# Kernel optimization log

Hardware: AMD Instinct MI355X
Metric: run time of the kernel (lower is better)

The kernel has to match this reference:

```python
import jax, jax.numpy as jnp
import numpy as np

H = 512
S = 65  # 64 board cells + appended constant 1


def _heads(y, wk, wq, wv):
    # y: [H, S]; wk/wq/wv: [3, H, H] -> atts: [3, S, H]
    def one(wk_i, wq_i, wv_i):
        k = wk_i @ y            # [H, S]
        q = wq_i @ y            # [H, S]
        v = wv_i @ y            # [H, S]
        sm = jax.nn.softmax(k.T @ q, axis=1)  # [S, S], softmax over dim=1
        return sm @ v.T         # [S, H]
    return jax.vmap(one)(wk, wq, wv)


def setup_inputs() -> dict:
    key = jax.random.key(0)
    ks = jax.random.split(key, 10)
    r = lambda k, s: jax.random.normal(k, s, dtype=jnp.float32)
    return {
        "inputs": r(ks[0], (1, 64)),
        "embedding": r(ks[1], (H, S)),
        "wq": r(ks[2], (3, 3, H, H)),
        "wk": r(ks[3], (3, 3, H, H)),
        "wv": r(ks[4], (3, 3, H, H)),
        "linear1": r(ks[5], (3 * H, H)),
        "linear2": r(ks[6], (3 * H, H)),
        "linear3": r(ks[7], (3 * H, 2 * H)),
        "linear4": r(ks[8], (2 * H, H)),
        "linear5": r(ks[9], (H, 64)),
    }


def reference(inputs, embedding, wq, wk, wv, linear1, linear2, linear3, linear4, linear5):
    x = jnp.concatenate([inputs[0], jnp.ones((1,), inputs.dtype)])  # [S]
    y = embedding * x  # [H, S] (broadcast over rows)

    # Layer 1 (3 heads)
    a1 = _heads(y, wk[0], wq[0], wv[0])  # [3, S, H]
    y = jax.nn.relu(jnp.concatenate([a1[0], a1[1], a1[2]], axis=1) @ linear1).T  # [H, S]

    # Layer 2 -- NOTE: original code cats att11, att12, att23 (a bug we preserve)
    a2 = _heads(y, wk[1], wq[1], wv[1])
    y = jax.nn.relu(jnp.concatenate([a1[0], a1[1], a2[2]], axis=1) @ linear2).T  # [H, S]

    # Layer 3 -- NOTE: original code cats att11, att12, att33 (preserved)
    a3 = _heads(y, wk[2], wq[2], wv[2])
    y = jax.nn.relu(jnp.concatenate([a1[0], a1[1], a3[2]], axis=1) @ linear3)[64]  # [2H]

    # dropout p=0.1 -> identity in eval mode
    y = jnp.tanh(y @ linear4)  # [H]
    score = y @ linear5        # [64]
    return score[None, :]      # [1, 64]
```

## Files before the change

kernel.cpp:

```cpp
#include <hip/hip_runtime.h>
#include <hip/hip_bf16.h>
#include <math.h>

#define H 512
#define S 65
#define SP 80
#define HS (H * S)
#define PHS (H * SP)
#define KS3 24
#define KS4 16


__global__ void scale_embed_kernel(const float* __restrict__ inp,
                                   const float* __restrict__ emb,
                                   float* __restrict__ yT) {
    int i = blockIdx.x * blockDim.x + threadIdx.x;
    if (i < PHS) {
        int s = i / H;
        int h = i % H;
        float v = 0.f;
        if (s < S) {
            float x = (s == 64) ? 1.0f : inp[s];
            v = emb[h * S + s] * x;
        }
        yT[i] = v;
    }
}

template <int COMBINE>
__global__ void __launch_bounds__(256, 1)
kqv_gemm_tiled(const float* __restrict__ wq,
               const float* __restrict__ wk,
               const float* __restrict__ wv,
               int mat0,
               const float* __restrict__ src,
               float* __restrict__ part) {
    int slot  = blockIdx.z;
    int which = blockIdx.y;
    int mat = mat0 + slot;
    const float* W = (which == 0 ? wk : (which == 1 ? wq : wv)) + (size_t)mat * H * H;

    int n0   = (blockIdx.x & 7) * 64;
    int kidx = blockIdx.x >> 3;

    __shared__ float Wt[64 * 64];
    __shared__ float As[SP * 64];

    int t  = threadIdx.x;
    int nq = t & 15;
    int g  = t >> 4;

    float4 acc[5];
#pragma unroll
    for (int r = 0; r < 5; ++r) acc[r] = make_float4(0.f, 0.f, 0.f, 0.f);

    for (int ch = 0; ch < 4; ++ch) {
        int kc0 = kidx * 256 + ch * 64;
#pragma unroll
        for (int c = 0; c < 4; ++c) {
            int f = c * 256 + t;
            int wn  = f >> 4;
            int kf4 = f & 15;
            float4 w4 = *(const float4*)(W + (size_t)(n0 + wn) * H + kc0 + 4 * kf4);
            int sw = ((wn >> 2) ^ (kf4 & 7));
            int base = (4 * kf4) * 64 + 4 * sw + (wn & 3);
            Wt[base      ] = w4.x;
            Wt[base +  64] = w4.y;
            Wt[base + 128] = w4.z;
            Wt[base + 192] = w4.w;
        }
#pragma unroll
        for (int c = 0; c < 5; ++c) {
            int f = c * 256 + t;
            int as  = f >> 4;
            int kf4 = f & 15;
            const float* addr = src + (size_t)as * H + kc0 + 4 * kf4;
            float4 v;
            if (COMBINE) {
                v = make_float4(0.f, 0.f, 0.f, 0.f);
#pragma unroll
                for (int p = 0; p < 6; ++p) {
                    float4 u = *(const float4*)(addr + (size_t)p * PHS);
                    v.x += u.x; v.y += u.y; v.z += u.z; v.w += u.w;
                }
                v.x = fmaxf(v.x, 0.f); v.y = fmaxf(v.y, 0.f);
                v.z = fmaxf(v.z, 0.f); v.w = fmaxf(v.w, 0.f);
            } else {
                v = *(const float4*)addr;
            }
            *(float4*)(&As[as * 64 + 4 * kf4]) = v;
        }
        __syncthreads();

#pragma unroll
        for (int k4 = 0; k4 < 16; ++k4) {
            int swc = 4 * (nq ^ (k4 & 7));
            float4 w0 = *(const float4*)(&Wt[(4 * k4 + 0) * 64 + swc]);
            float4 w1 = *(const float4*)(&Wt[(4 * k4 + 1) * 64 + swc]);
            float4 w2 = *(const float4*)(&Wt[(4 * k4 + 2) * 64 + swc]);
            float4 w3 = *(const float4*)(&Wt[(4 * k4 + 3) * 64 + swc]);
#pragma unroll
            for (int r = 0; r < 5; ++r) {
                float4 a = *(const float4*)(&As[(g + 16 * r) * 64 + 4 * k4]);
                acc[r].x = fmaf(a.x, w0.x, acc[r].x);
                acc[r].y = fmaf(a.x, w0.y, acc[r].y);
                acc[r].z = fmaf(a.x, w0.z, acc[r].z);
                acc[r].w = fmaf(a.x, w0.w, acc[r].w);
                acc[r].x = fmaf(a.y, w1.x, acc[r].x);
                acc[r].y = fmaf(a.y, w1.y, acc[r].y);
                acc[r].z = fmaf(a.y, w1.z, acc[r].z);
                acc[r].w = fmaf(a.y, w1.w, acc[r].w);
                acc[r].x = fmaf(a.z, w2.x, acc[r].x);
                acc[r].y = fmaf(a.z, w2.y, acc[r].y);
                acc[r].z = fmaf(a.z, w2.z, acc[r].z);
                acc[r].w = fmaf(a.z, w2.w, acc[r].w);
                acc[r].x = fmaf(a.w, w3.x, acc[r].x);
                acc[r].y = fmaf(a.w, w3.y, acc[r].y);
                acc[r].z = fmaf(a.w, w3.z, acc[r].z);
                acc[r].w = fmaf(a.w, w3.w, acc[r].w);
            }
        }
        __syncthreads();
    }

    float* P = part + (size_t)((slot * 3 + which) * 2 + kidx) * PHS;
#pragma unroll
    for (int r = 0; r < 5; ++r) {
        *(float4*)(P + (size_t)(g + 16 * r) * H + n0 + 4 * nq) = acc[r];
    }
}

__device__ __forceinline__ float score_part(const float* __restrict__ Q0,
                                            const float* __restrict__ Q1,
                                            const float* __restrict__ ka,
                                            int b, int t) {
    const float4* q0 = (const float4*)(Q0 + (size_t)b * H) + t * 32;
    const float4* q1 = (const float4*)(Q1 + (size_t)b * H) + t * 32;
    const float4* kl = (const float4*)ka + t * 32;
    float4 c0 = {0,0,0,0}, c1 = {0,0,0,0};
#pragma unroll
    for (int u = 0; u < 32; u += 2) {
        float4 qa = q0[u], qb = q1[u], k0 = kl[u];
        float4 qc = q0[u+1], qd = q1[u+1], k1 = kl[u+1];
        c0.x = fmaf(k0.x, qa.x + qb.x, c0.x);
        c0.y = fmaf(k0.y, qa.y + qb.y, c0.y);
        c0.z = fmaf(k0.z, qa.z + qb.z, c0.z);
        c0.w = fmaf(k0.w, qa.w + qb.w, c0.w);
        c1.x = fmaf(k1.x, qc.x + qd.x, c1.x);
        c1.y = fmaf(k1.y, qc.y + qd.y, c1.y);
        c1.z = fmaf(k1.z, qc.z + qd.z, c1.z);
        c1.w = fmaf(k1.w, qc.w + qd.w, c1.w);
    }
    return ((c0.x + c0.y) + (c0.z + c0.w)) + ((c1.x + c1.y) + (c1.z + c1.w));
}

__global__ void attn_kernel(const float* __restrict__ kqvp,
                            float* __restrict__ att) {
    int a = blockIdx.x;
    int slot = blockIdx.y;
    int tid = threadIdx.x;

    const float* base = kqvp + (size_t)slot * 6 * PHS;
    const float* K0 = base;
    const float* K1 = base + PHS;
    const float* Q0 = base + 2 * (size_t)PHS;
    const float* Q1 = base + 3 * (size_t)PHS;
    const float* V0 = base + 4 * (size_t)PHS;
    const float* V1 = base + 5 * (size_t)PHS;
    float* ao = att + (size_t)slot * PHS + (size_t)a * H;

    __shared__ float ka[H];
    __shared__ float sp[4 * 65];
    __shared__ float smv[S];
    __shared__ float p[S];

    ka[tid]       = K0[(size_t)a * H + tid]       + K1[(size_t)a * H + tid];
    ka[tid + 256] = K0[(size_t)a * H + tid + 256] + K1[(size_t)a * H + tid + 256];
    __syncthreads();

    {
        int b = tid & 63;
        int t = tid >> 6;
        sp[t * 65 + b] = score_part(Q0, Q1, ka, b, t);
        if (tid < 4) sp[tid * 65 + 64] = score_part(Q0, Q1, ka, 64, tid);
    }
    __syncthreads();

    if (tid < S) {
        smv[tid] = (sp[tid] + sp[65 + tid]) + (sp[130 + tid] + sp[195 + tid]);
    }
    __syncthreads();

    float maxv = -INFINITY;
    for (int i = 0; i < S; ++i) maxv = fmaxf(maxv, smv[i]);
    float sum = 0.0f;
    for (int i = 0; i < S; ++i) sum += expf(smv[i] - maxv);
    float inv = 1.0f / sum;
    if (tid < S) p[tid] = expf(smv[tid] - maxv) * inv;
    __syncthreads();

#pragma unroll
    for (int rep = 0; rep < 2; ++rep) {
        int hh = tid + rep * 256;
        float a0 = 0.f, a1 = 0.f;
#pragma unroll 4
        for (int b = 0; b < 64; b += 2) {
            a0 = fmaf(p[b    ], V0[(size_t)(b    ) * H + hh] + V1[(size_t)(b    ) * H + hh], a0);
            a1 = fmaf(p[b + 1], V0[(size_t)(b + 1) * H + hh] + V1[(size_t)(b + 1) * H + hh], a1);
        }
        a0 = fmaf(p[64], V0[(size_t)64 * H + hh] + V1[(size_t)64 * H + hh], a0);
        ao[hh] = a0 + a1;
    }
}

__global__ void mega_lin_kernel(const float* __restrict__ att1,
                                const float* __restrict__ lin1,
                                const float* __restrict__ lin2,
                                const float* __restrict__ lin3,
                                float* __restrict__ plin1,
                                float* __restrict__ plin2,
                                float* __restrict__ tpart) {
    int bx = blockIdx.x;
    int tid = threadIdx.x;

    if (bx < 1300) {
        const float* att;
        const float* L;
        float* dst;
        int x, seg;
        if (bx < 780) {
            seg = bx / 130; x = bx - seg * 130;
            att = att1 + (size_t)(seg >> 1) * PHS;
            L   = lin1 + (size_t)(seg * 256) * H;
            dst = plin1 + (size_t)seg * PHS;
        } else {
            int b2 = bx - 780;
            seg = b2 / 130; x = b2 - seg * 130;
            att = att1 + (size_t)(seg >> 1) * PHS;
            L   = lin2 + (size_t)(seg * 256) * H;
            dst = plin2 + (size_t)seg * PHS;
        }
        int i = x * 256 + tid;
        int s = i / H;
        int h = i % H;
        const float* row = att + (size_t)s * H + (seg & 1) * 256;
        const float* Lh = L + h;
        float a0 = 0.f, a1 = 0.f, a2 = 0.f, a3 = 0.f;
        for (int j = 0; j < 256; j += 4) {
            a0 = fmaf(row[j + 0], Lh[(size_t)(j + 0) * H], a0);
            a1 = fmaf(row[j + 1], Lh[(size_t)(j + 1) * H], a1);
            a2 = fmaf(row[j + 2], Lh[(size_t)(j + 2) * H], a2);
            a3 = fmaf(row[j + 3], Lh[(size_t)(j + 3) * H], a3);
        }
        dst[(size_t)s * H + h] = (a0 + a1) + (a2 + a3);
    } else {
        int idx = bx - 1300;
        int j2 = (idx & 3) * 256 + tid;
        int ks = idx >> 2;
        const float* row = att1 + (size_t)(ks >> 3) * PHS + (size_t)64 * H;
        int j0 = (ks & 7) * 64;
        int jbase = ks * 64;
        float a0 = 0.f, a1 = 0.f, a2 = 0.f, a3 = 0.f;
        for (int j = 0; j < 64; j += 4) {
            a0 = fmaf(row[j0 + j + 0], lin3[(size_t)(jbase + j + 0) * 1024 + j2], a0);
            a1 = fmaf(row[j0 + j + 1], lin3[(size_t)(jbase + j + 1) * 1024 + j2], a1);
            a2 = fmaf(row[j0 + j + 2], lin3[(size_t)(jbase + j + 2) * 1024 + j2], a2);
            a3 = fmaf(row[j0 + j + 3], lin3[(size_t)(jbase + j + 3) * 1024 + j2], a3);
        }
        tpart[ks * 1024 + j2] = (a0 + a1) + (a2 + a3);
    }
}

__global__ void lin2c_kernel(const float* __restrict__ att2,
                             const float* __restrict__ lin2,
                             float* __restrict__ plin2) {
    int seg = 4 + blockIdx.y;
    int i = blockIdx.x * 256 + threadIdx.x;
    int s = i / H;
    int h = i % H;
    const float* row = att2 + (size_t)s * H + (seg & 1) * 256;
    const float* Lh = lin2 + (size_t)(seg * 256) * H + h;
    float a0 = 0.f, a1 = 0.f, a2 = 0.f, a3 = 0.f;
    for (int j = 0; j < 256; j += 4) {
        a0 = fmaf(row[j + 0], Lh[(size_t)(j + 0) * H], a0);
        a1 = fmaf(row[j + 1], Lh[(size_t)(j + 1) * H], a1);
        a2 = fmaf(row[j + 2], Lh[(size_t)(j + 2) * H], a2);
        a3 = fmaf(row[j + 3], Lh[(size_t)(j + 3) * H], a3);
    }
    plin2[(size_t)seg * PHS + (size_t)s * H + h] = (a0 + a1) + (a2 + a3);
}

__global__ void attn3_lin3c_kernel(const float* __restrict__ kqvp,
                                   const float* __restrict__ lin3,
                                   float* __restrict__ tpart) {
    int tid = threadIdx.x;
    int ks  = 16 + blockIdx.y;
    int j2  = blockIdx.x * 256 + tid;
    int j0  = (ks & 7) * 64;

    const float* K0 = kqvp;
    const float* K1 = kqvp + PHS;
    const float* Q0 = kqvp + 2 * (size_t)PHS;
    const float* Q1 = kqvp + 3 * (size_t)PHS;
    const float* V0 = kqvp + 4 * (size_t)PHS;
    const float* V1 = kqvp + 5 * (size_t)PHS;

    __shared__ float ka[H];
    __shared__ float sp[4 * 65];
    __shared__ float smv[S];
    __shared__ float p[S];
    __shared__ float att_s[64];

    ka[tid]       = K0[(size_t)64 * H + tid]       + K1[(size_t)64 * H + tid];
    ka[tid + 256] = K0[(size_t)64 * H + tid + 256] + K1[(size_t)64 * H + tid + 256];
    __syncthreads();

    {
        int b = tid & 63;
        int t = tid >> 6;
        sp[t * 65 + b] = score_part(Q0, Q1, ka, b, t);
        if (tid < 4) sp[tid * 65 + 64] = score_part(Q0, Q1, ka, 64, tid);
    }
    __syncthreads();

    if (tid < S) {
        smv[tid] = (sp[tid] + sp[65 + tid]) + (sp[130 + tid] + sp[195 + tid]);
    }
    __syncthreads();

    float maxv = -INFINITY;
    for (int i = 0; i < S; ++i) maxv = fmaxf(maxv, smv[i]);
    float sum = 0.0f;
    for (int i = 0; i < S; ++i) sum += expf(smv[i] - maxv);
    float inv = 1.0f / sum;
    if (tid < S) p[tid] = expf(smv[tid] - maxv) * inv;
    __syncthreads();

    if (tid < 64) {
        int hh = j0 + tid;
        float a0 = 0.f, a1 = 0.f;
#pragma unroll 4
        for (int b = 0; b < 64; b += 2) {
            a0 = fmaf(p[b    ], V0[(size_t)(b    ) * H + hh] + V1[(size_t)(b    ) * H + hh], a0);
            a1 = fmaf(p[b + 1], V0[(size_t)(b + 1) * H + hh] + V1[(size_t)(b + 1) * H + hh], a1);
        }
        a0 = fmaf(p[64], V0[(size_t)64 * H + hh] + V1[(size_t)64 * H + hh], a0);
        att_s[tid] = a0 + a1;
    }
    __syncthreads();

    int jbase = ks * 64;
    float a0 = 0.f, a1 = 0.f, a2 = 0.f, a3 = 0.f;
    for (int j = 0; j < 64; j += 4) {
        a0 = fmaf(att_s[j + 0], lin3[(size_t)(jbase + j + 0) * 1024 + j2], a0);
        a1 = fmaf(att_s[j + 1], lin3[(size_t)(jbase + j + 1) * 1024 + j2], a1);
        a2 = fmaf(att_s[j + 2], lin3[(size_t)(jbase + j + 2) * 1024 + j2], a2);
        a3 = fmaf(att_s[j + 3], lin3[(size_t)(jbase + j + 3) * 1024 + j2], a3);
    }
    tpart[ks * 1024 + j2] = (a0 + a1) + (a2 + a3);
}

__global__ void lin4_partial_kernel(const float* __restrict__ tpart,
                                    const float* __restrict__ lin4,
                                    float* __restrict__ upart) {
    __shared__ float tl[64];
    int hh = blockIdx.x * 256 + threadIdx.x;
    int ks = blockIdx.y;
    int j2base = ks * 64;

    if (threadIdx.x < 64) {
        int j2 = j2base + threadIdx.x;
        float s = 0.f;
#pragma unroll
        for (int p = 0; p < KS3; ++p) s += tpart[p * 1024 + j2];
        tl[threadIdx.x] = fmaxf(s, 0.f);
    }
    __syncthreads();

    float a0 = 0.f, a1 = 0.f, a2 = 0.f, a3 = 0.f;
    for (int j = 0; j < 64; j += 4) {
        a0 = fmaf(tl[j + 0], lin4[(size_t)(j2base + j + 0) * H + hh], a0);
        a1 = fmaf(tl[j + 1], lin4[(size_t)(j2base + j + 1) * H + hh], a1);
        a2 = fmaf(tl[j + 2], lin4[(size_t)(j2base + j + 2) * H + hh], a2);
        a3 = fmaf(tl[j + 3], lin4[(size_t)(j2base + j + 3) * H + hh], a3);
    }
    upart[ks * H + hh] = (a0 + a1) + (a2 + a3);
}

__global__ void final_out_kernel(const float* __restrict__ upart,
                                 const float* __restrict__ lin5,
                                 float* __restrict__ out) {
    __shared__ float u[H];
    __shared__ float pr[8][64];
    int tid = threadIdx.x;

    {
        float s = 0.f;
#pragma unroll
        for (int p = 0; p < KS4; ++p) s += upart[p * H + tid];
        u[tid] = tanhf(s);
    }
    __syncthreads();

    int o  = tid & 63;
    int sl = tid >> 6;
    float acc = 0.f;
    int h0 = sl * 64;
#pragma unroll 8
    for (int j = 0; j < 64; ++j) {
        acc = fmaf(u[h0 + j], lin5[(h0 + j) * 64 + o], acc);
    }
    pr[sl][o] = acc;
    __syncthreads();

    if (tid < 64) {
        float s = 0.f;
#pragma unroll
        for (int p = 0; p < 8; ++p) s += pr[p][tid];
        out[tid] = s;
    }
}

extern "C" void kernel_launch(void* const* d_in, const int* in_sizes, int n_in,
                              void* d_out, int out_size, void* d_ws, size_t ws_size,
                              hipStream_t stream) {
    const float* inputs  = (const float*)d_in[0];
    const float* emb     = (const float*)d_in[1];
    const float* wq      = (const float*)d_in[2];
    const float* wk      = (const float*)d_in[3];
    const float* wv      = (const float*)d_in[4];
    const float* linear1 = (const float*)d_in[5];
    const float* linear2 = (const float*)d_in[6];
    const float* linear3 = (const float*)d_in[7];
    const float* linear4 = (const float*)d_in[8];
    const float* linear5 = (const float*)d_in[9];
    float* out = (float*)d_out;

    float* ws    = (float*)d_ws;
    float* y     = ws;
    float* kqvp  = y     + PHS;
    float* att1  = kqvp  + 18 * PHS;
    float* att2  = att1  + 3 * PHS;
    float* plin1 = att2  + PHS;
    float* plin2 = plin1 + 6 * PHS;
    float* tpart = plin2 + 6 * PHS;
    float* upart = tpart + KS3 * 1024;

    const int nbp = PHS / 256;

    scale_embed_kernel<<<nbp, 256, 0, stream>>>(inputs, emb, y);

    kqv_gemm_tiled<0><<<dim3(16, 3, 3), 256, 0, stream>>>(wq, wk, wv, 0, y, kqvp);
    attn_kernel<<<dim3(S, 3), 256, 0, stream>>>(kqvp, att1);
    mega_lin_kernel<<<1364, 256, 0, stream>>>(att1, linear1, linear2, linear3,
                                              plin1, plin2, tpart);

    kqv_gemm_tiled<1><<<dim3(16, 3, 1), 256, 0, stream>>>(wq, wk, wv, 5, plin1, kqvp);
    attn_kernel<<<dim3(S, 1), 256, 0, stream>>>(kqvp, att2);
    lin2c_kernel<<<dim3(130, 2), 256, 0, stream>>>(att2, linear2, plin2);

    kqv_gemm_tiled<1><<<dim3(16, 3, 1), 256, 0, stream>>>(wq, wk, wv, 8, plin2, kqvp);
    attn3_lin3c_kernel<<<dim3(4, 8), 256, 0, stream>>>(kqvp, linear3, tpart);

    lin4_partial_kernel<<<dim3(2, KS4), 256, 0, stream>>>(tpart, linear4, upart);
    final_out_kernel<<<1, 512, 0, stream>>>(upart, linear5, out);
}
```

Before: 260.4 us.

## Retile KQV GEMM, register-block linear projections, split out combine+relu kernel

```diff
diff --git a/kernel.cpp b/kernel.cpp
--- a/kernel.cpp
+++ b/kernel.cpp
@@ -27,107 +27,96 @@
     }
 }
 
-template <int COMBINE>
+__device__ __forceinline__ void mac4(float4& c, float ax, float ay, float az,
+                                     float aw, const float4& w0, const float4& w1,
+                                     const float4& w2, const float4& w3) {
+    c.x = fmaf(ax, w0.x, c.x); c.y = fmaf(ax, w0.y, c.y);
+    c.z = fmaf(ax, w0.z, c.z); c.w = fmaf(ax, w0.w, c.w);
+    c.x = fmaf(ay, w1.x, c.x); c.y = fmaf(ay, w1.y, c.y);
+    c.z = fmaf(ay, w1.z, c.z); c.w = fmaf(ay, w1.w, c.w);
+    c.x = fmaf(az, w2.x, c.x); c.y = fmaf(az, w2.y, c.y);
+    c.z = fmaf(az, w2.z, c.z); c.w = fmaf(az, w2.w, c.w);
+    c.x = fmaf(aw, w3.x, c.x); c.y = fmaf(aw, w3.y, c.y);
+    c.z = fmaf(aw, w3.z, c.z); c.w = fmaf(aw, w3.w, c.w);
+}
+
 __global__ void __launch_bounds__(256, 1)
 kqv_gemm_tiled(const float* __restrict__ wq,
                const float* __restrict__ wk,
                const float* __restrict__ wv,
                int mat0,
-               const float* __restrict__ src,
+               const float* __restrict__ yT,
                float* __restrict__ part) {
     int slot  = blockIdx.z;
     int which = blockIdx.y;
     int mat = mat0 + slot;
     const float* W = (which == 0 ? wk : (which == 1 ? wq : wv)) + (size_t)mat * H * H;
 
-    int n0   = (blockIdx.x & 7) * 64;
-    int kidx = blockIdx.x >> 3;
-
-    __shared__ float Wt[64 * 64];
-    __shared__ float As[SP * 64];
+    int n0   = (blockIdx.x & 15) * 32;
+    int kidx = blockIdx.x >> 4;
+
+    __shared__ float Wt[64 * 32];
+    __shared__ float As[SP * 68];
 
     int t  = threadIdx.x;
-    int nq = t & 15;
-    int g  = t >> 4;
-
-    float4 acc[5];
-#pragma unroll
-    for (int r = 0; r < 5; ++r) acc[r] = make_float4(0.f, 0.f, 0.f, 0.f);
+    int nq = t & 7;
+    int g  = t >> 3;
+    bool r2 = (g < 16);
+
+    float4 acc0 = {0,0,0,0}, acc1 = {0,0,0,0}, acc2 = {0,0,0,0};
 
     for (int ch = 0; ch < 4; ++ch) {
         int kc0 = kidx * 256 + ch * 64;
 #pragma unroll
-        for (int c = 0; c < 4; ++c) {
+        for (int c = 0; c < 2; ++c) {
             int f = c * 256 + t;
             int wn  = f >> 4;
             int kf4 = f & 15;
             float4 w4 = *(const float4*)(W + (size_t)(n0 + wn) * H + kc0 + 4 * kf4);
             int sw = ((wn >> 2) ^ (kf4 & 7));
-            int base = (4 * kf4) * 64 + 4 * sw + (wn & 3);
-            Wt[base      ] = w4.x;
-            Wt[base +  64] = w4.y;
-            Wt[base + 128] = w4.z;
-            Wt[base + 192] = w4.w;
+            int base = (4 * kf4) * 32 + 4 * sw + (wn & 3);
+            Wt[base     ] = w4.x;
+            Wt[base + 32] = w4.y;
+            Wt[base + 64] = w4.z;
+            Wt[base + 96] = w4.w;
         }
 #pragma unroll
         for (int c = 0; c < 5; ++c) {
             int f = c * 256 + t;
             int as  = f >> 4;
             int kf4 = f & 15;
-            const float* addr = src + (size_t)as * H + kc0 + 4 * kf4;
-            float4 v;
-            if (COMBINE) {
-                v = make_float4(0.f, 0.f, 0.f, 0.f);
-#pragma unroll
-                for (int p = 0; p < 6; ++p) {
-                    float4 u = *(const float4*)(addr + (size_t)p * PHS);
-                    v.x += u.x; v.y += u.y; v.z += u.z; v.w += u.w;
-                }
-                v.x = fmaxf(v.x, 0.f); v.y = fmaxf(v.y, 0.f);
-                v.z = fmaxf(v.z, 0.f); v.w = fmaxf(v.w, 0.f);
-            } else {
-                v = *(const float4*)addr;
-            }
-            *(float4*)(&As[as * 64 + 4 * kf4]) = v;
+            *(float4*)(&As[as * 68 + 4 * kf4]) =
+                *(const float4*)(yT + (size_t)as * H + kc0 + 4 * kf4);
         }
         __syncthreads();
 
 #pragma unroll
         for (int k4 = 0; k4 < 16; ++k4) {
             int swc = 4 * (nq ^ (k4 & 7));
-            float4 w0 = *(const float4*)(&Wt[(4 * k4 + 0) * 64 + swc]);
-            float4 w1 = *(const float4*)(&Wt[(4 * k4 + 1) * 64 + swc]);
-            float4 w2 = *(const float4*)(&Wt[(4 * k4 + 2) * 64 + swc]);
-            float4 w3 = *(const float4*)(&Wt[(4 * k4 + 3) * 64 + swc]);
-#pragma unroll
-            for (int r = 0; r < 5; ++r) {
-                float4 a = *(const float4*)(&As[(g + 16 * r) * 64 + 4 * k4]);
-                acc[r].x = fmaf(a.x, w0.x, acc[r].x);
-                acc[r].y = fmaf(a.x, w0.y, acc[r].y);
-                acc[r].z = fmaf(a.x, w0.z, acc[r].z);
-                acc[r].w = fmaf(a.x, w0.w, acc[r].w);
-                acc[r].x = fmaf(a.y, w1.x, acc[r].x);
-                acc[r].y = fmaf(a.y, w1.y, acc[r].y);
-                acc[r].z = fmaf(a.y, w1.z, acc[r].z);
-                acc[r].w = fmaf(a.y, w1.w, acc[r].w);
-                acc[r].x = fmaf(a.z, w2.x, acc[r].x);
-                acc[r].y = fmaf(a.z, w2.y, acc[r].y);
-                acc[r].z = fmaf(a.z, w2.z, acc[r].z);
-                acc[r].w = fmaf(a.z, w2.w, acc[r].w);
-                acc[r].x = fmaf(a.w, w3.x, acc[r].x);
-                acc[r].y = fmaf(a.w, w3.y, acc[r].y);
-                acc[r].z = fmaf(a.w, w3.z, acc[r].z);
-                acc[r].w = fmaf(a.w, w3.w, acc[r].w);
+            float4 w0 = *(const float4*)(&Wt[(4 * k4 + 0) * 32 + swc]);
+            float4 w1 = *(const float4*)(&Wt[(4 * k4 + 1) * 32 + swc]);
+            float4 w2 = *(const float4*)(&Wt[(4 * k4 + 2) * 32 + swc]);
+            float4 w3 = *(const float4*)(&Wt[(4 * k4 + 3) * 32 + swc]);
+            {
+                float4 a = *(const float4*)(&As[g * 68 + 4 * k4]);
+                mac4(acc0, a.x, a.y, a.z, a.w, w0, w1, w2, w3);
             }
+            {
+                float4 a = *(const float4*)(&As[(g + 32) * 68 + 4 * k4]);
+                mac4(acc1, a.x, a.y, a.z, a.w, w0, w1, w2, w3);
+            }
+            if (r2) {
+                float4 a = *(const float4*)(&As[(g + 64) * 68 + 4 * k4]);
+                mac4(acc2, a.x, a.y, a.z, a.w, w0, w1, w2, w3);
+            }
         }
         __syncthreads();
     }
 
     float* P = part + (size_t)((slot * 3 + which) * 2 + kidx) * PHS;
-#pragma unroll
-    for (int r = 0; r < 5; ++r) {
-        *(float4*)(P + (size_t)(g + 16 * r) * H + n0 + 4 * nq) = acc[r];
-    }
+    *(float4*)(P + (size_t)g * H + n0 + 4 * nq) = acc0;
+    *(float4*)(P + (size_t)(g + 32) * H + n0 + 4 * nq) = acc1;
+    if (r2) *(float4*)(P + (size_t)(g + 64) * H + n0 + 4 * nq) = acc2;
 }
 
 __device__ __forceinline__ float score_part(const float* __restrict__ Q0,
@@ -213,6 +202,60 @@
     }
 }
 
+__device__ __forceinline__ void lin4row_dev(const float* __restrict__ att,
+                                            int col0,
+                                            const float* __restrict__ L,
+                                            float* __restrict__ dst,
+                                            int s0, int tid) {
+    __shared__ float Ar[4 * 256];
+    __shared__ float4 red[4 * 128];
+
+    {
+        int rr = tid >> 6;
+        int cc = tid & 63;
+        *(float4*)(&Ar[rr * 256 + cc * 4]) =
+            *(const float4*)(att + (size_t)(s0 + rr) * H + col0 + cc * 4);
+    }
+    __syncthreads();
+
+    int h4 = (tid & 127) * 4;
+    int jh = tid >> 7;
+    const float* Lj = L + (size_t)(jh * 128) * H + h4;
+    const float* A0 = Ar + jh * 128;
+
+    float4 c0 = {0,0,0,0}, c1 = {0,0,0,0}, c2 = {0,0,0,0}, c3 = {0,0,0,0};
+#pragma unroll 8
+    for (int j = 0; j < 128; ++j) {
+        float4 L4 = *(const float4*)(Lj + (size_t)j * H);
+        float a0 = A0[j], a1 = A0[256 + j], a2 = A0[512 + j], a3 = A0[768 + j];
+        c0.x = fmaf(a0, L4.x, c0.x); c0.y = fmaf(a0, L4.y, c0.y);
+        c0.z = fmaf(a0, L4.z, c0.z); c0.w = fmaf(a0, L4.w, c0.w);
+        c1.x = fmaf(a1, L4.x, c1.x); c1.y = fmaf(a1, L4.y, c1.y);
+        c1.z = fmaf(a1, L4.z, c1.z); c1.w = fmaf(a1, L4.w, c1.w);
+        c2.x = fmaf(a2, L4.x, c2.x); c2.y = fmaf(a2, L4.y, c2.y);
+        c2.z = fmaf(a2, L4.z, c2.z); c2.w = fmaf(a2, L4.w, c2.w);
+        c3.x = fmaf(a3, L4.x, c3.x); c3.y = fmaf(a3, L4.y, c3.y);
+        c3.z = fmaf(a3, L4.z, c3.z); c3.w = fmaf(a3, L4.w, c3.w);
+    }
+
+    if (jh == 1) {
+        int x = tid & 127;
+        red[x] = c0; red[128 + x] = c1; red[256 + x] = c2; red[384 + x] = c3;
+    }
+    __syncthreads();
+    if (jh == 0) {
+        float4 r0 = red[tid], r1 = red[128 + tid], r2 = red[256 + tid], r3 = red[384 + tid];
+        c0.x += r0.x; c0.y += r0.y; c0.z += r0.z; c0.w += r0.w;
+        c1.x += r1.x; c1.y += r1.y; c1.z += r1.z; c1.w += r1.w;
+        c2.x += r2.x; c2.y += r2.y; c2.z += r2.z; c2.w += r2.w;
+        c3.x += r3.x; c3.y += r3.y; c3.z += r3.z; c3.w += r3.w;
+        *(float4*)(dst + (size_t)(s0 + 0) * H + h4) = c0;
+        *(float4*)(dst + (size_t)(s0 + 1) * H + h4) = c1;
+        *(float4*)(dst + (size_t)(s0 + 2) * H + h4) = c2;
+        *(float4*)(dst + (size_t)(s0 + 3) * H + h4) = c3;
+    }
+}
+
 __global__ void mega_lin_kernel(const float* __restrict__ att1,
                                 const float* __restrict__ lin1,
                                 const float* __restrict__ lin2,
@@ -223,38 +266,25 @@
     int bx = blockIdx.x;
     int tid = threadIdx.x;
 
-    if (bx < 1300) {
+    if (bx < 170) {
+        int seg = bx / 17;
+        int p   = bx % 17;
         const float* att;
         const float* L;
         float* dst;
-        int x, seg;
-        if (bx < 780) {
-            seg = bx / 130; x = bx - seg * 130;
+        if (seg < 6) {
             att = att1 + (size_t)(seg >> 1) * PHS;
             L   = lin1 + (size_t)(seg * 256) * H;
             dst = plin1 + (size_t)seg * PHS;
         } else {
-            int b2 = bx - 780;
-            seg = b2 / 130; x = b2 - seg * 130;
-            att = att1 + (size_t)(seg >> 1) * PHS;
-            L   = lin2 + (size_t)(seg * 256) * H;
-            dst = plin2 + (size_t)seg * PHS;
-        }
-        int i = x * 256 + tid;
-        int s = i / H;
-        int h = i % H;
-        const float* row = att + (size_t)s * H + (seg & 1) * 256;
-        const float* Lh = L + h;
-        float a0 = 0.f, a1 = 0.f, a2 = 0.f, a3 = 0.f;
-        for (int j = 0; j < 256; j += 4) {
-            a0 = fmaf(row[j + 0], Lh[(size_t)(j + 0) * H], a0);
-            a1 = fmaf(row[j + 1], Lh[(size_t)(j + 1) * H], a1);
-            a2 = fmaf(row[j + 2], Lh[(size_t)(j + 2) * H], a2);
-            a3 = fmaf(row[j + 3], Lh[(size_t)(j + 3) * H], a3);
-        }
-        dst[(size_t)s * H + h] = (a0 + a1) + (a2 + a3);
+            int s2 = seg - 6;
+            att = att1 + (size_t)(s2 >> 1) * PHS;
+            L   = lin2 + (size_t)(s2 * 256) * H;
+            dst = plin2 + (size_t)s2 * PHS;
+        }
+        lin4row_dev(att, (seg & 1) * 256, L, dst, p * 4, tid);
     } else {
-        int idx = bx - 1300;
+        int idx = bx - 170;
         int j2 = (idx & 3) * 256 + tid;
         int ks = idx >> 2;
         const float* row = att1 + (size_t)(ks >> 3) * PHS + (size_t)64 * H;
@@ -274,20 +304,19 @@
 __global__ void lin2c_kernel(const float* __restrict__ att2,
                              const float* __restrict__ lin2,
                              float* __restrict__ plin2) {
-    int seg = 4 + blockIdx.y;
+    int seg = 4 + blockIdx.x / 17;
+    int p   = blockIdx.x % 17;
+    lin4row_dev(att2, (seg & 1) * 256, lin2 + (size_t)(seg * 256) * H,
+                plin2 + (size_t)seg * PHS, p * 4, threadIdx.x);
+}
+
+__global__ void combine6_relu_kernel(const float* __restrict__ part,
+                                     float* __restrict__ yT) {
     int i = blockIdx.x * 256 + threadIdx.x;
-    int s = i / H;
-    int h = i % H;
-    const float* row = att2 + (size_t)s * H + (seg & 1) * 256;
-    const float* Lh = lin2 + (size_t)(seg * 256) * H + h;
-    float a0 = 0.f, a1 = 0.f, a2 = 0.f, a3 = 0.f;
-    for (int j = 0; j < 256; j += 4) {
-        a0 = fmaf(row[j + 0], Lh[(size_t)(j + 0) * H], a0);
-        a1 = fmaf(row[j + 1], Lh[(size_t)(j + 1) * H], a1);
-        a2 = fmaf(row[j + 2], Lh[(size_t)(j + 2) * H], a2);
-        a3 = fmaf(row[j + 3], Lh[(size_t)(j + 3) * H], a3);
-    }
-    plin2[(size_t)seg * PHS + (size_t)s * H + h] = (a0 + a1) + (a2 + a3);
+    float s = 0.f;
+#pragma unroll
+    for (int p = 0; p < 6; ++p) s += part[(size_t)p * PHS + i];
+    yT[i] = fmaxf(s, 0.0f);
 }
 
 __global__ void attn3_lin3c_kernel(const float* __restrict__ kqvp,
@@ -446,20 +475,23 @@
     float* tpart = plin2 + 6 * PHS;
     float* upart = tpart + KS3 * 1024;
 
+    const int nb  = HS / 256;
     const int nbp = PHS / 256;
 
     scale_embed_kernel<<<nbp, 256, 0, stream>>>(inputs, emb, y);
 
-    kqv_gemm_tiled<0><<<dim3(16, 3, 3), 256, 0, stream>>>(wq, wk, wv, 0, y, kqvp);
+    kqv_gemm_tiled<<<dim3(32, 3, 3), 256, 0, stream>>>(wq, wk, wv, 0, y, kqvp);
     attn_kernel<<<dim3(S, 3), 256, 0, stream>>>(kqvp, att1);
-    mega_lin_kernel<<<1364, 256, 0, stream>>>(att1, linear1, linear2, linear3,
-                                              plin1, plin2, tpart);
-
-    kqv_gemm_tiled<1><<<dim3(16, 3, 1), 256, 0, stream>>>(wq, wk, wv, 5, plin1, kqvp);
+    mega_lin_kernel<<<234, 256, 0, stream>>>(att1, linear1, linear2, linear3,
+                                             plin1, plin2, tpart);
+    combine6_relu_kernel<<<nb, 256, 0, stream>>>(plin1, y);
+
+    kqv_gemm_tiled<<<dim3(32, 3, 1), 256, 0, stream>>>(wq, wk, wv, 5, y, kqvp);
     attn_kernel<<<dim3(S, 1), 256, 0, stream>>>(kqvp, att2);
-    lin2c_kernel<<<dim3(130, 2), 256, 0, stream>>>(att2, linear2, plin2);
-
-    kqv_gemm_tiled<1><<<dim3(16, 3, 1), 256, 0, stream>>>(wq, wk, wv, 8, plin2, kqvp);
+    lin2c_kernel<<<34, 256, 0, stream>>>(att2, linear2, plin2);
+    combine6_relu_kernel<<<nb, 256, 0, stream>>>(plin2, y);
+
+    kqv_gemm_tiled<<<dim3(32, 3, 1), 256, 0, stream>>>(wq, wk, wv, 8, y, kqvp);
     attn3_lin3c_kernel<<<dim3(4, 8), 256, 0, stream>>>(kqvp, linear3, tpart);
 
     lin4_partial_kernel<<<dim3(2, KS4), 256, 0, stream>>>(tpart, linear4, upart);
```

After: 254.8 us. 2.1% less time.
